# Kernel tuning notes

Measured on AMD Instinct MI355X. Metric: run time of the kernel, lower is better.

## Reference

```python
import jax, jax.numpy as jnp
import numpy as np
from jax import lax

HIDDEN = 256      # hidden_dim
LATENT = 128      # latent_dim
VOCAB = 32000     # vocab_size
MAX_LEN = 64      # max_len (stack capacity guard, as in original)
MAX_STEPS = 128   # fixed step budget for the decode stack machine
N_NODES = 511     # complete binary tree, depth 9


def _linear_params(key, fan_in, fan_out):
    k1, k2 = jax.random.split(key)
    s = 1.0 / np.sqrt(fan_in)
    W = jax.random.uniform(k1, (fan_out, fan_in), minval=-s, maxval=s, dtype=jnp.float32)
    b = jax.random.uniform(k2, (fan_out,), minval=-s, maxval=s, dtype=jnp.float32)
    return W, b


def setup_inputs() -> dict:
    key = jax.random.key(0)
    ks = jax.random.split(key, 10)
    embed = jax.random.normal(ks[0], (VOCAB, HIDDEN), dtype=jnp.float32)
    Wpar, bpar = _linear_params(ks[1], 3 * HIDDEN, HIDDEN)
    Wmu, bmu = _linear_params(ks[2], HIDDEN, LATENT)
    Wlv, blv = _linear_params(ks[3], HIDDEN, LATENT)
    W1, b1 = _linear_params(ks[4], LATENT, HIDDEN)
    W2, b2 = _linear_params(ks[5], HIDDEN, HIDDEN + 1)
    Wl, bl = _linear_params(ks[6], HIDDEN, VOCAB)
    Wp, bp = _linear_params(ks[7], HIDDEN, 2 * LATENT + VOCAB)
    values = jax.random.randint(ks[8], (N_NODES,), 0, VOCAB)
    idx = np.arange(N_NODES)
    left = np.where(2 * idx + 1 < N_NODES, 2 * idx + 1, -1).astype(np.int32)
    right = np.where(2 * idx + 2 < N_NODES, 2 * idx + 2, -1).astype(np.int32)
    eps = jax.random.normal(ks[9], (LATENT,), dtype=jnp.float32)
    return dict(embed=embed, Wpar=Wpar, bpar=bpar, Wmu=Wmu, bmu=bmu,
                Wlv=Wlv, blv=blv, W1=W1, b1=b1, W2=W2, b2=b2,
                Wl=Wl, bl=bl, Wp=Wp, bp=bp, eps=eps,
                values=jnp.asarray(values), left=jnp.asarray(left), right=jnp.asarray(right))


def reference(embed, Wpar, bpar, Wmu, bmu, Wlv, blv, W1, b1, W2, b2,
              Wl, bl, Wp, bp, eps, values, left, right):
    # ---------- encode: bottom-up over tree stored as index arrays ----------
    emb = embed[values]  # [N, H], one gather for all node embeddings

    def enc_step(h, i):
        v = emb[i]
        li = jnp.maximum(left[i], 0)
        ri = jnp.maximum(right[i], 0)
        cat = jnp.concatenate([v, h[li], h[ri]])          # [3H]
        hp = cat @ Wpar.T + bpar                           # parent combine
        hi = jnp.where(left[i] < 0, v, hp)                 # leaf -> embedding
        return h.at[i].set(hi), None

    h0 = jnp.zeros((values.shape[0], HIDDEN), dtype=embed.dtype)
    # children have larger index than parents -> process in descending order
    h, _ = lax.scan(enc_step, h0, jnp.arange(values.shape[0] - 1, -1, -1))
    root = h[0]
    mu = root @ Wmu.T + bmu
    logvar = root @ Wlv.T + blv
    z = mu + eps * jnp.exp(0.5 * logvar)                   # reparameterize

    # ---------- decode: stack machine with fixed step budget ----------
    V, L = VOCAB, LATENT
    stack0 = jnp.zeros((MAX_LEN, L), dtype=z.dtype).at[0].set(z)
    out0 = jnp.zeros((MAX_STEPS, V), dtype=z.dtype)

    def dec_step(state, _):
        stack, sp, out, op = state
        active = sp > 0
        idx = jnp.maximum(sp - 1, 0)
        node = stack[idx]                                  # pop
        hmid = jax.nn.leaky_relu(node @ W1.T + b1, 0.2)
        co = hmid @ W2.T + b2                              # [H+1]; co[0] = gate
        is_parent = (co[0] > 0) & (sp - 1 <= MAX_LEN - 2) & active

        def parent_fn(_):
            dec = co[1:] @ Wp.T + bp                       # [V + 2L]
            value = dec[:V]
            ll = dec[V:V + L]
            rl = dec[V + L:]
            # original appends llatent then rlatent -> rlatent on top
            st = stack.at[idx].set(ll).at[idx + 1].set(rl)
            return value, st, sp + 1

        def leaf_fn(_):
            return co[1:] @ Wl.T + bl, stack, sp - 1

        value, st, nsp = lax.cond(is_parent, parent_fn, leaf_fn, None)
        m = active.astype(z.dtype)
        out = out.at[op].add(m * value)                    # rows written once
        stack = jnp.where(active, st, stack)
        sp = jnp.where(active, nsp, sp)
        op = op + active.astype(op.dtype)
        return (stack, sp, out, op), None

    init = (stack0, jnp.int32(1), out0, jnp.int32(0))
    (_, _, out, _), _ = lax.scan(dec_step, init, None, length=MAX_STEPS)
    return out, mu, logvar
```

## Files before the change

### kernel.cpp

```cpp
#include <hip/hip_runtime.h>

#define HID 256
#define LAT 128
#define VOC 32000
#define NSTEP 128

__global__ __launch_bounds__(256)
void prep_kernel(const float* __restrict__ Wp, const float* __restrict__ W2,
                 const float* __restrict__ b2, const float* __restrict__ bp,
                 const float* __restrict__ Wpar,
                 const float* __restrict__ Wmu, const float* __restrict__ Wlv,
                 float* __restrict__ Wcomb, float* __restrict__ bcomb,
                 float* __restrict__ Wq_par, float* __restrict__ Wq_mu,
                 float* __restrict__ Wq_lv, float* __restrict__ Wq_w2) {
    const int b = blockIdx.x;
    const int t = threadIdx.x;
    if (b < 256) {
        const int o = b, k = t;
        __shared__ float wpt_s[256];
        __shared__ float red_s[4];
        wpt_s[k] = Wp[(size_t)(VOC + o) * HID + k];
        __syncthreads();
        float acc = 0.f;
#pragma unroll 8
        for (int j = 0; j < 256; j++)
            acc += wpt_s[j] * W2[(size_t)(1 + j) * HID + k];
        Wcomb[(size_t)o * HID + k] = acc;
        float p = wpt_s[k] * b2[1 + k];
        p += __shfl_xor(p, 1);  p += __shfl_xor(p, 2);  p += __shfl_xor(p, 4);
        p += __shfl_xor(p, 8);  p += __shfl_xor(p, 16); p += __shfl_xor(p, 32);
        if ((k & 63) == 0) red_s[k >> 6] = p;
        __syncthreads();
        if (k == 0) bcomb[o] = bp[VOC + o] + red_s[0] + red_s[1] + red_s[2] + red_s[3];
    } else if (b < 448) {
        const int k4 = b - 256;
        const float4 v = *(const float4*)(Wpar + (size_t)t * 768 + 4 * k4);
        ((float4*)Wq_par)[k4 * 256 + t] = v;
    } else if (b < 512) {
        const int k4 = b - 448;
        const int r = t & 127;
        const float* src = (t < 128 ? Wmu : Wlv) + (size_t)r * HID + 4 * k4;
        const float4 v = *(const float4*)src;
        ((float4*)(t < 128 ? Wq_mu : Wq_lv))[k4 * 128 + r] = v;
    } else {
        const int k4 = b - 512;
        const float4 v = *(const float4*)(W2 + (size_t)(1 + t) * HID + 4 * k4);
        ((float4*)Wq_w2)[k4 * 256 + t] = v;
    }
}

__global__ __launch_bounds__(256)
void enc2(const float* __restrict__ embed, const int* __restrict__ values,
          const float* __restrict__ Wq, const float* __restrict__ bpar,
          float* __restrict__ h, int base) {
    const int i = base + blockIdx.x;
    const int t = threadIdx.x;
    __shared__ __align__(16) float cat[768];
    __shared__ float hc[2][256];
    const float bv = bpar[t];
    const float4* wq = (const float4*)Wq + t;

    for (int s = 0; s < 2; s++) {
        const int c = 2 * i + 1 + s;
        cat[t] = embed[(size_t)values[c] * HID + t];
        const int g1 = 2 * c + 1, g2 = 2 * c + 2;
        cat[256 + t] = (g1 >= 255) ? embed[(size_t)values[g1] * HID + t]
                                   : h[(size_t)g1 * HID + t];
        cat[512 + t] = (g2 >= 255) ? embed[(size_t)values[g2] * HID + t]
                                   : h[(size_t)g2 * HID + t];
        __syncthreads();
        float acc = bv;
        const float4* c4 = (const float4*)cat;
#pragma unroll 8
        for (int k4 = 0; k4 < 192; k4++) {
            const float4 w = wq[k4 * 256];
            const float4 cc = c4[k4];
            acc += w.x * cc.x + w.y * cc.y + w.z * cc.z + w.w * cc.w;
        }
        hc[s][t] = acc;
        h[(size_t)c * HID + t] = acc;
        __syncthreads();
    }
    cat[t] = embed[(size_t)values[i] * HID + t];
    cat[256 + t] = hc[0][t];
    cat[512 + t] = hc[1][t];
    __syncthreads();
    float acc = bv;
    const float4* c4 = (const float4*)cat;
#pragma unroll 8
    for (int k4 = 0; k4 < 192; k4++) {
        const float4 w = wq[k4 * 256];
        const float4 cc = c4[k4];
        acc += w.x * cc.x + w.y * cc.y + w.z * cc.z + w.w * cc.w;
    }
    h[(size_t)i * HID + t] = acc;
}

__global__ __launch_bounds__(256)
void enc_final(const float* __restrict__ embed, const int* __restrict__ values,
               const float* __restrict__ Wq, const float* __restrict__ bpar,
               const float* __restrict__ h,
               const float* __restrict__ Wq_mu, const float* __restrict__ bmu,
               const float* __restrict__ Wq_lv, const float* __restrict__ blv,
               const float* __restrict__ eps,
               float* __restrict__ out, float* __restrict__ z) {
    const int t = threadIdx.x;
    __shared__ __align__(16) float cat[768];
    __shared__ float hc[2][256];
    __shared__ __align__(16) float r0[256];
    __shared__ float mu_s[128], lv_s[128];
    const float bv = bpar[t];
    const float4* wq = (const float4*)Wq + t;

    for (int s = 0; s < 2; s++) {
        const int c = 1 + s;
        cat[t] = embed[(size_t)values[c] * HID + t];
        cat[256 + t] = h[(size_t)(2 * c + 1) * HID + t];
        cat[512 + t] = h[(size_t)(2 * c + 2) * HID + t];
        __syncthreads();
        float acc = bv;
        const float4* c4 = (const float4*)cat;
#pragma unroll 8
        for (int k4 = 0; k4 < 192; k4++) {
            const float4 w = wq[k4 * 256];
            const float4 cc = c4[k4];
            acc += w.x * cc.x + w.y * cc.y + w.z * cc.z + w.w * cc.w;
        }
        hc[s][t] = acc;
        __syncthreads();
    }
    cat[t] = embed[(size_t)values[0] * HID + t];
    cat[256 + t] = hc[0][t];
    cat[512 + t] = hc[1][t];
    __syncthreads();
    {
        float acc = bv;
        const float4* c4 = (const float4*)cat;
#pragma unroll 8
        for (int k4 = 0; k4 < 192; k4++) {
            const float4 w = wq[k4 * 256];
            const float4 cc = c4[k4];
            acc += w.x * cc.x + w.y * cc.y + w.z * cc.z + w.w * cc.w;
        }
        r0[t] = acc;
    }
    __syncthreads();
    const int r = t & 127;
    const float4* wqh = (const float4*)(t < 128 ? Wq_mu : Wq_lv) + r;
    float acc2 = (t < 128) ? bmu[r] : blv[r];
    const float4* r4 = (const float4*)r0;
#pragma unroll 8
    for (int k4 = 0; k4 < 64; k4++) {
        const float4 w = wqh[k4 * 128];
        const float4 cc = r4[k4];
        acc2 += w.x * cc.x + w.y * cc.y + w.z * cc.z + w.w * cc.w;
    }
    if (t < 128) { out[(size_t)NSTEP * VOC + r] = acc2;       mu_s[r] = acc2; }
    else         { out[(size_t)NSTEP * VOC + 128 + r] = acc2; lv_s[r] = acc2; }
    __syncthreads();
    if (t < 128) z[t] = mu_s[t] + eps[t] * expf(0.5f * lv_s[t]);
}

__global__ __launch_bounds__(512, 2)
void recur_kernel(const float* W1, const float* b1,
                  const float* W2, const float* b2,
                  const float* Wcomb, const float* bcomb,
                  const float* z,
                  float* Hrec, int* rowflag) {
    const int t = threadIdx.x;
    const int o = t >> 1;
    const int hk = t & 1;
    __shared__ __align__(16) float stack_s[64 * 128];
    __shared__ __align__(16) float hmid_s[256];

    float4 w1r[16];
#pragma unroll
    for (int j = 0; j < 16; j++)
        w1r[j] = *(const float4*)(W1 + (size_t)o * 128 + hk * 64 + 4 * j);
    float4 wcr[32];
#pragma unroll
    for (int j = 0; j < 32; j++)
        wcr[j] = *(const float4*)(Wcomb + (size_t)o * 256 + hk * 128 + 4 * j);

    const float b1o = b1[o];
    const float bco = bcomb[o];
    const float b20 = b2[0];
    const int l64 = t & 63;
    const float4 w2q = *(const float4*)(W2 + 4 * l64);

    if (t < 128) stack_s[t] = z[t];
    int sp = 1, op = 0;
    unsigned long long pm0 = 0ULL, pm1 = 0ULL;
    __syncthreads();

    for (int step = 0; step < NSTEP; step++) {
        if (sp <= 0) break;
        const int idx = sp - 1;

        const float* np = stack_s + idx * 128 + hk * 64;
        float a = 0.f;
#pragma unroll
        for (int j = 0; j < 16; j++) {
            const float4 v = *(const float4*)(np + 4 * j);
            a += w1r[j].x * v.x + w1r[j].y * v.y + w1r[j].z * v.z + w1r[j].w * v.w;
        }
        a += __shfl_xor(a, 1);
        if (hk == 0) {
            float pre = a + b1o;
            pre = pre > 0.f ? pre : 0.2f * pre;
            hmid_s[o] = pre;
            Hrec[(size_t)op * HID + o] = pre;
        }
        __syncthreads();

        const float4 hq = *(const float4*)(hmid_s + 4 * l64);
        float c = w2q.x * hq.x + w2q.y * hq.y + w2q.z * hq.z + w2q.w * hq.w;
        c += __shfl_xor(c, 1);  c += __shfl_xor(c, 2);  c += __shfl_xor(c, 4);
        c += __shfl_xor(c, 8);  c += __shfl_xor(c, 16); c += __shfl_xor(c, 32);
        const bool par = ((c + b20) > 0.f) && (sp <= 63);

        if (par) {
            const float* hp = hmid_s + hk * 128;
            float s = 0.f;
#pragma unroll
            for (int j = 0; j < 32; j++) {
                const float4 v = *(const float4*)(hp + 4 * j);
                s += wcr[j].x * v.x + wcr[j].y * v.y + wcr[j].z * v.z + wcr[j].w * v.w;
            }
            s += __shfl_xor(s, 1);
            if (hk == 0)
                stack_s[(idx + (o >> 7)) * 128 + (o & 127)] = s + bco;
            if (op < 64) pm0 |= (1ULL << op); else pm1 |= (1ULL << (op - 64));
            sp += 1;
        } else {
            sp -= 1;
        }
        op++;
        __syncthreads();
    }

    if (t < 128) {
        int f = -1;
        if (t < op) f = (t < 64) ? (int)((pm0 >> t) & 1) : (int)((pm1 >> (t - 64)) & 1);
        rowflag[t] = f;
    }
}

__global__ __launch_bounds__(256)
void co1_kernel(const float* __restrict__ Hrec, const float* __restrict__ Wq_w2,
                const float* __restrict__ b2, float* __restrict__ Co1) {
    const int r = blockIdx.x;
    const int c = threadIdx.x;
    __shared__ __align__(16) float hs[256];
    hs[c] = Hrec[(size_t)r * HID + c];
    __syncthreads();
    float acc = b2[1 + c];
    const float4* wq = (const float4*)Wq_w2 + c;
    const float4* h4 = (const float4*)hs;
#pragma unroll 8
    for (int k4 = 0; k4 < 64; k4++) {
        const float4 a = wq[k4 * 256];
        const float4 hv = h4[k4];
        acc += a.x * hv.x + a.y * hv.y + a.z * hv.z + a.w * hv.w;
    }
    Co1[(size_t)r * HID + c] = acc;
}

__global__ __launch_bounds__(256, 1)
void value_kernel(const float* __restrict__ Co1, const int* __restrict__ rowflag,
                  const float* __restrict__ Wl, const float* __restrict__ bl,
                  const float* __restrict__ Wp, const float* __restrict__ bp,
                  float* __restrict__ out) {
    const int m = blockIdx.y;
    const int t = threadIdx.x;
    const int v = blockIdx.x * 256 + t;
    __shared__ int list_s[128];
    __shared__ int zlist_s[128];
    __shared__ int nn_s, nz_s;
    if (t == 0) {
        int n = 0, znum = 0;
        for (int r = 0; r < 128; r++) {
            const int f = rowflag[r];
            if (f == m) list_s[n++] = r;
            else if (m == 0 && f == -1) zlist_s[znum++] = r;
        }
        nn_s = n; nz_s = znum;
    }
    __syncthreads();
    const int n = nn_s;
    const float* Wx = m ? Wp : Wl;
    const float* bx = m ? bp : bl;
    const float bv = bx[v];
    const float4* w4 = (const float4*)(Wx + (size_t)v * HID);

    for (int rc = 0; rc < n; rc += 32) {
        const int nr = min(32, n - rc);
        float acc[32];
#pragma unroll
        for (int rr = 0; rr < 32; rr++) acc[rr] = 0.f;
        for (int kc = 0; kc < 4; kc++) {
            float4 w[16];
#pragma unroll
            for (int i = 0; i < 16; i++) w[i] = w4[kc * 16 + i];
            for (int rr = 0; rr < nr; rr++) {
                const int row = __builtin_amdgcn_readfirstlane(list_s[rc + rr]);
                const float* cp = Co1 + (size_t)row * HID + kc * 64;
                float s = 0.f;
#pragma unroll
                for (int i = 0; i < 16; i++) {
                    const float4 c4 = *(const float4*)(cp + 4 * i);
                    s += w[i].x * c4.x + w[i].y * c4.y + w[i].z * c4.z + w[i].w * c4.w;
                }
                acc[rr] += s;
            }
        }
        for (int rr = 0; rr < nr; rr++) {
            const int row = __builtin_amdgcn_readfirstlane(list_s[rc + rr]);
            out[(size_t)row * VOC + v] = acc[rr] + bv;
        }
    }
    if (m == 0) {
        const int nz = nz_s;
        for (int i = 0; i < nz; i++) {
            const int row = __builtin_amdgcn_readfirstlane(zlist_s[i]);
            out[(size_t)row * VOC + v] = 0.f;
        }
    }
}

extern "C" void kernel_launch(void* const* d_in, const int* in_sizes, int n_in,
                              void* d_out, int out_size, void* d_ws, size_t ws_size,
                              hipStream_t stream) {
    const float* embed = (const float*)d_in[0];
    const float* Wpar  = (const float*)d_in[1];
    const float* bpar  = (const float*)d_in[2];
    const float* Wmu   = (const float*)d_in[3];
    const float* bmu   = (const float*)d_in[4];
    const float* Wlv   = (const float*)d_in[5];
    const float* blv   = (const float*)d_in[6];
    const float* W1    = (const float*)d_in[7];
    const float* b1    = (const float*)d_in[8];
    const float* W2    = (const float*)d_in[9];
    const float* b2    = (const float*)d_in[10];
    const float* Wl    = (const float*)d_in[11];
    const float* bl    = (const float*)d_in[12];
    const float* Wp    = (const float*)d_in[13];
    const float* bp    = (const float*)d_in[14];
    const float* eps   = (const float*)d_in[15];
    const int*  values = (const int*)d_in[16];

    float* ws = (float*)d_ws;
    float* h       = ws;
    float* z       = ws + 65280;
    float* Wcomb   = ws + 65408;
    float* bcomb   = ws + 130944;
    float* Hrec    = ws + 131200;
    float* Co1     = ws + 163968;
    int*   rowflag = (int*)(ws + 196736);
    float* Wq_par  = ws + 196864;
    float* Wq_mu   = ws + 393472;
    float* Wq_lv   = ws + 426240;
    float* Wq_w2   = ws + 459008;
    float* out = (float*)d_out;

    prep_kernel<<<576, 256, 0, stream>>>(Wp, W2, b2, bp, Wpar, Wmu, Wlv,
                                         Wcomb, bcomb, Wq_par, Wq_mu, Wq_lv, Wq_w2);

    enc2<<<64, 256, 0, stream>>>(embed, values, Wq_par, bpar, h, 63);
    enc2<<<16, 256, 0, stream>>>(embed, values, Wq_par, bpar, h, 15);
    enc2<<< 4, 256, 0, stream>>>(embed, values, Wq_par, bpar, h,  3);
    enc_final<<<1, 256, 0, stream>>>(embed, values, Wq_par, bpar, h,
                                     Wq_mu, bmu, Wq_lv, blv, eps, out, z);

    recur_kernel<<<1, 512, 0, stream>>>(W1, b1, W2, b2, Wcomb, bcomb, z, Hrec, rowflag);

    co1_kernel<<<128, 256, 0, stream>>>(Hrec, Wq_w2, b2, Co1);
    value_kernel<<<dim3(125, 2), 256, 0, stream>>>(Co1, rowflag, Wl, bl, Wp, bp, out);
}
```

Before: 297.0 us.

## Widen encoder and prep blocks with split-K partial sums across more threads

The encoder kernels now launch 1024 threads per block. Both child nodes are computed at the same time, and each dot product is split across K groups whose partial sums are reduced through shared memory. The prep kernel uses 512-thread blocks, halving the j-loop for Wcomb and handling two float4 columns per block for the weight transposes. The goal is to shorten the serial latency of the small-grid encoder launches, which leave most of the GPU idle, at the cost of extra syncs and shared-memory reductions.

```diff
diff --git a/kernel.cpp b/kernel.cpp
--- a/kernel.cpp
+++ b/kernel.cpp
@@ -5,7 +5,7 @@
 #define VOC 32000
 #define NSTEP 128
 
-__global__ __launch_bounds__(256)
+__global__ __launch_bounds__(512)
 void prep_kernel(const float* __restrict__ Wp, const float* __restrict__ W2,
                  const float* __restrict__ b2, const float* __restrict__ bp,
                  const float* __restrict__ Wpar,
@@ -16,87 +16,111 @@
     const int b = blockIdx.x;
     const int t = threadIdx.x;
     if (b < 256) {
-        const int o = b, k = t;
+        const int o = b;
+        const int k = t & 255, jh = t >> 8;
         __shared__ float wpt_s[256];
+        __shared__ float part_s[2][256];
         __shared__ float red_s[4];
-        wpt_s[k] = Wp[(size_t)(VOC + o) * HID + k];
+        if (t < 256) wpt_s[t] = Wp[(size_t)(VOC + o) * HID + t];
         __syncthreads();
         float acc = 0.f;
 #pragma unroll 8
-        for (int j = 0; j < 256; j++)
-            acc += wpt_s[j] * W2[(size_t)(1 + j) * HID + k];
-        Wcomb[(size_t)o * HID + k] = acc;
-        float p = wpt_s[k] * b2[1 + k];
-        p += __shfl_xor(p, 1);  p += __shfl_xor(p, 2);  p += __shfl_xor(p, 4);
-        p += __shfl_xor(p, 8);  p += __shfl_xor(p, 16); p += __shfl_xor(p, 32);
-        if ((k & 63) == 0) red_s[k >> 6] = p;
+        for (int j = 0; j < 128; j++)
+            acc += wpt_s[jh * 128 + j] * W2[(size_t)(1 + jh * 128 + j) * HID + k];
+        part_s[jh][k] = acc;
+        if (t < 256) {
+            float p = wpt_s[k] * b2[1 + k];
+            p += __shfl_xor(p, 1);  p += __shfl_xor(p, 2);  p += __shfl_xor(p, 4);
+            p += __shfl_xor(p, 8);  p += __shfl_xor(p, 16); p += __shfl_xor(p, 32);
+            if ((k & 63) == 0) red_s[k >> 6] = p;
+        }
         __syncthreads();
-        if (k == 0) bcomb[o] = bp[VOC + o] + red_s[0] + red_s[1] + red_s[2] + red_s[3];
-    } else if (b < 448) {
-        const int k4 = b - 256;
-        const float4 v = *(const float4*)(Wpar + (size_t)t * 768 + 4 * k4);
-        ((float4*)Wq_par)[k4 * 256 + t] = v;
-    } else if (b < 512) {
-        const int k4 = b - 448;
-        const int r = t & 127;
-        const float* src = (t < 128 ? Wmu : Wlv) + (size_t)r * HID + 4 * k4;
-        const float4 v = *(const float4*)src;
-        ((float4*)(t < 128 ? Wq_mu : Wq_lv))[k4 * 128 + r] = v;
+        if (t < 256) Wcomb[(size_t)o * HID + k] = part_s[0][k] + part_s[1][k];
+        if (t == 0) bcomb[o] = bp[VOC + o] + red_s[0] + red_s[1] + red_s[2] + red_s[3];
+    } else if (b < 352) {
+        const int k4 = (b - 256) * 2 + (t >> 8);
+        const int r = t & 255;
+        ((float4*)Wq_par)[k4 * 256 + r] = *(const float4*)(Wpar + (size_t)r * 768 + 4 * k4);
+    } else if (b < 384) {
+        const int k4 = (b - 352) * 2 + (t >> 8);
+        const int r = t & 127, sel = (t >> 7) & 1;
+        const float* src = (sel ? Wlv : Wmu) + (size_t)r * HID + 4 * k4;
+        ((float4*)(sel ? Wq_lv : Wq_mu))[k4 * 128 + r] = *(const float4*)src;
     } else {
-        const int k4 = b - 512;
-        const float4 v = *(const float4*)(W2 + (size_t)(1 + t) * HID + 4 * k4);
-        ((float4*)Wq_w2)[k4 * 256 + t] = v;
-    }
-}
-
-__global__ __launch_bounds__(256)
+        const int k4 = (b - 384) * 2 + (t >> 8);
+        const int r = t & 255;
+        ((float4*)Wq_w2)[k4 * 256 + r] = *(const float4*)(W2 + (size_t)(1 + r) * HID + 4 * k4);
+    }
+}
+
+__global__ __launch_bounds__(1024)
 void enc2(const float* __restrict__ embed, const int* __restrict__ values,
           const float* __restrict__ Wq, const float* __restrict__ bpar,
           float* __restrict__ h, int base) {
     const int i = base + blockIdx.x;
     const int t = threadIdx.x;
-    __shared__ __align__(16) float cat[768];
-    __shared__ float hc[2][256];
-    const float bv = bpar[t];
-    const float4* wq = (const float4*)Wq + t;
-
-    for (int s = 0; s < 2; s++) {
-        const int c = 2 * i + 1 + s;
-        cat[t] = embed[(size_t)values[c] * HID + t];
-        const int g1 = 2 * c + 1, g2 = 2 * c + 2;
-        cat[256 + t] = (g1 >= 255) ? embed[(size_t)values[g1] * HID + t]
-                                   : h[(size_t)g1 * HID + t];
-        cat[512 + t] = (g2 >= 255) ? embed[(size_t)values[g2] * HID + t]
-                                   : h[(size_t)g2 * HID + t];
-        __syncthreads();
-        float acc = bv;
-        const float4* c4 = (const float4*)cat;
-#pragma unroll 8
-        for (int k4 = 0; k4 < 192; k4++) {
-            const float4 w = wq[k4 * 256];
+    const int o = t & 255;
+    const int g = t >> 8;
+    const int cid = g & 1, kh = g >> 1;
+    __shared__ __align__(16) float cat[2][768];
+    __shared__ float part[4][256];
+    __shared__ __align__(16) float pcat[768];
+
+    const int c0n = 2 * i + 1;
+    for (int q = t; q < 1536; q += 1024) {
+        const int cc = (q >= 768);
+        const int e = q - cc * 768;
+        const int node = c0n + cc;
+        const int seg = e >> 8, idx = e & 255;
+        float v;
+        if (seg == 0) v = embed[(size_t)values[node] * HID + idx];
+        else {
+            const int ch = 2 * node + seg;
+            v = (ch >= 255) ? embed[(size_t)values[ch] * HID + idx]
+                            : h[(size_t)ch * HID + idx];
+        }
+        cat[cc][e] = v;
+    }
+    __syncthreads();
+    {
+        const float4* wq = (const float4*)Wq + o;
+        const float4* c4 = (const float4*)cat[cid] + kh * 96;
+        float acc = 0.f;
+#pragma unroll 16
+        for (int k4 = 0; k4 < 96; k4++) {
+            const float4 w = wq[(size_t)(kh * 96 + k4) * 256];
             const float4 cc = c4[k4];
             acc += w.x * cc.x + w.y * cc.y + w.z * cc.z + w.w * cc.w;
         }
-        hc[s][t] = acc;
-        h[(size_t)c * HID + t] = acc;
-        __syncthreads();
-    }
-    cat[t] = embed[(size_t)values[i] * HID + t];
-    cat[256 + t] = hc[0][t];
-    cat[512 + t] = hc[1][t];
-    __syncthreads();
-    float acc = bv;
-    const float4* c4 = (const float4*)cat;
-#pragma unroll 8
-    for (int k4 = 0; k4 < 192; k4++) {
-        const float4 w = wq[k4 * 256];
-        const float4 cc = c4[k4];
-        acc += w.x * cc.x + w.y * cc.y + w.z * cc.z + w.w * cc.w;
-    }
-    h[(size_t)i * HID + t] = acc;
-}
-
-__global__ __launch_bounds__(256)
+        part[g][o] = acc;
+    }
+    __syncthreads();
+    if (t < 512) {
+        const int c = t >> 8;
+        pcat[256 + (c << 8) + o] = part[c][o] + part[c + 2][o] + bpar[o];
+    } else if (t < 768) {
+        const int idx = t & 255;
+        pcat[idx] = embed[(size_t)values[i] * HID + idx];
+    }
+    __syncthreads();
+    {
+        const float4* wq = (const float4*)Wq + o;
+        const float4* c4 = (const float4*)pcat + g * 48;
+        float acc = 0.f;
+#pragma unroll 16
+        for (int k4 = 0; k4 < 48; k4++) {
+            const float4 w = wq[(size_t)(g * 48 + k4) * 256];
+            const float4 cc = c4[k4];
+            acc += w.x * cc.x + w.y * cc.y + w.z * cc.z + w.w * cc.w;
+        }
+        part[g][o] = acc;
+    }
+    __syncthreads();
+    if (t < 256)
+        h[(size_t)i * HID + t] = part[0][t] + part[1][t] + part[2][t] + part[3][t] + bpar[t];
+}
+
+__global__ __launch_bounds__(1024)
 void enc_final(const float* __restrict__ embed, const int* __restrict__ values,
                const float* __restrict__ Wq, const float* __restrict__ bpar,
                const float* __restrict__ h,
@@ -105,58 +129,81 @@
                const float* __restrict__ eps,
                float* __restrict__ out, float* __restrict__ z) {
     const int t = threadIdx.x;
-    __shared__ __align__(16) float cat[768];
-    __shared__ float hc[2][256];
+    const int o = t & 255;
+    const int g = t >> 8;
+    const int cid = g & 1, kh = g >> 1;
+    __shared__ __align__(16) float cat[2][768];
+    __shared__ float part[4][256];
+    __shared__ __align__(16) float pcat[768];
     __shared__ __align__(16) float r0[256];
     __shared__ float mu_s[128], lv_s[128];
-    const float bv = bpar[t];
-    const float4* wq = (const float4*)Wq + t;
-
-    for (int s = 0; s < 2; s++) {
-        const int c = 1 + s;
-        cat[t] = embed[(size_t)values[c] * HID + t];
-        cat[256 + t] = h[(size_t)(2 * c + 1) * HID + t];
-        cat[512 + t] = h[(size_t)(2 * c + 2) * HID + t];
-        __syncthreads();
-        float acc = bv;
-        const float4* c4 = (const float4*)cat;
-#pragma unroll 8
-        for (int k4 = 0; k4 < 192; k4++) {
-            const float4 w = wq[k4 * 256];
+
+    for (int q = t; q < 1536; q += 1024) {
+        const int cc = (q >= 768);
+        const int e = q - cc * 768;
+        const int node = 1 + cc;
+        const int seg = e >> 8, idx = e & 255;
+        cat[cc][e] = (seg == 0) ? embed[(size_t)values[node] * HID + idx]
+                                : h[(size_t)(2 * node + seg) * HID + idx];
+    }
+    __syncthreads();
+    {
+        const float4* wq = (const float4*)Wq + o;
+        const float4* c4 = (const float4*)cat[cid] + kh * 96;
+        float acc = 0.f;
+#pragma unroll 16
+        for (int k4 = 0; k4 < 96; k4++) {
+            const float4 w = wq[(size_t)(kh * 96 + k4) * 256];
             const float4 cc = c4[k4];
             acc += w.x * cc.x + w.y * cc.y + w.z * cc.z + w.w * cc.w;
         }
-        hc[s][t] = acc;
-        __syncthreads();
-    }
-    cat[t] = embed[(size_t)values[0] * HID + t];
-    cat[256 + t] = hc[0][t];
-    cat[512 + t] = hc[1][t];
+        part[g][o] = acc;
+    }
+    __syncthreads();
+    if (t < 512) {
+        const int c = t >> 8;
+        pcat[256 + (c << 8) + o] = part[c][o] + part[c + 2][o] + bpar[o];
+    } else if (t < 768) {
+        const int idx = t & 255;
+        pcat[idx] = embed[(size_t)values[0] * HID + idx];
+    }
     __syncthreads();
     {
-        float acc = bv;
-        const float4* c4 = (const float4*)cat;
-#pragma unroll 8
-        for (int k4 = 0; k4 < 192; k4++) {
-            const float4 w = wq[k4 * 256];
+        const float4* wq = (const float4*)Wq + o;
+        const float4* c4 = (const float4*)pcat + g * 48;
+        float acc = 0.f;
+#pragma unroll 16
+        for (int k4 = 0; k4 < 48; k4++) {
+            const float4 w = wq[(size_t)(g * 48 + k4) * 256];
             const float4 cc = c4[k4];
             acc += w.x * cc.x + w.y * cc.y + w.z * cc.z + w.w * cc.w;
         }
-        r0[t] = acc;
-    }
-    __syncthreads();
-    const int r = t & 127;
-    const float4* wqh = (const float4*)(t < 128 ? Wq_mu : Wq_lv) + r;
-    float acc2 = (t < 128) ? bmu[r] : blv[r];
-    const float4* r4 = (const float4*)r0;
-#pragma unroll 8
-    for (int k4 = 0; k4 < 64; k4++) {
-        const float4 w = wqh[k4 * 128];
-        const float4 cc = r4[k4];
-        acc2 += w.x * cc.x + w.y * cc.y + w.z * cc.z + w.w * cc.w;
-    }
-    if (t < 128) { out[(size_t)NSTEP * VOC + r] = acc2;       mu_s[r] = acc2; }
-    else         { out[(size_t)NSTEP * VOC + 128 + r] = acc2; lv_s[r] = acc2; }
+        part[g][o] = acc;
+    }
+    __syncthreads();
+    if (t < 256)
+        r0[t] = part[0][t] + part[1][t] + part[2][t] + part[3][t] + bpar[t];
+    __syncthreads();
+    {
+        const int r = o & 127;
+        const float4* wqh = (const float4*)(o < 128 ? Wq_mu : Wq_lv) + r;
+        const float4* r4 = (const float4*)r0 + g * 16;
+        float acc = 0.f;
+#pragma unroll 16
+        for (int k4 = 0; k4 < 16; k4++) {
+            const float4 w = wqh[(size_t)(g * 16 + k4) * 128];
+            const float4 cc = r4[k4];
+            acc += w.x * cc.x + w.y * cc.y + w.z * cc.z + w.w * cc.w;
+        }
+        part[g][o] = acc;
+    }
+    __syncthreads();
+    if (t < 256) {
+        const int r = t & 127;
+        float v = part[0][t] + part[1][t] + part[2][t] + part[3][t];
+        if (t < 128) { v += bmu[r]; out[(size_t)NSTEP * VOC + r] = v;       mu_s[r] = v; }
+        else         { v += blv[r]; out[(size_t)NSTEP * VOC + 128 + r] = v; lv_s[r] = v; }
+    }
     __syncthreads();
     if (t < 128) z[t] = mu_s[t] + eps[t] * expf(0.5f * lv_s[t]);
 }
@@ -363,14 +410,14 @@
     float* Wq_w2   = ws + 459008;
     float* out = (float*)d_out;
 
-    prep_kernel<<<576, 256, 0, stream>>>(Wp, W2, b2, bp, Wpar, Wmu, Wlv,
+    prep_kernel<<<416, 512, 0, stream>>>(Wp, W2, b2, bp, Wpar, Wmu, Wlv,
                                          Wcomb, bcomb, Wq_par, Wq_mu, Wq_lv, Wq_w2);
 
-    enc2<<<64, 256, 0, stream>>>(embed, values, Wq_par, bpar, h, 63);
-    enc2<<<16, 256, 0, stream>>>(embed, values, Wq_par, bpar, h, 15);
-    enc2<<< 4, 256, 0, stream>>>(embed, values, Wq_par, bpar, h,  3);
-    enc_final<<<1, 256, 0, stream>>>(embed, values, Wq_par, bpar, h,
-                                     Wq_mu, bmu, Wq_lv, blv, eps, out, z);
+    enc2<<<64, 1024, 0, stream>>>(embed, values, Wq_par, bpar, h, 63);
+    enc2<<<16, 1024, 0, stream>>>(embed, values, Wq_par, bpar, h, 15);
+    enc2<<< 4, 1024, 0, stream>>>(embed, values, Wq_par, bpar, h,  3);
+    enc_final<<<1, 1024, 0, stream>>>(embed, values, Wq_par, bpar, h,
+                                      Wq_mu, bmu, Wq_lv, blv, eps, out, z);
 
     recur_kernel<<<1, 512, 0, stream>>>(W1, b1, W2, b2, Wcomb, bcomb, z, Hrec, rowflag);
 
```

Measured after the change: 283.2 us. -4.6%, faster.
